# Kernel tuning notes

Measured on AMD Instinct MI355X. Metric: run time of the kernel, lower is better.

The kernel has to match this reference:

```python
import jax, jax.numpy as jnp
import numpy as np

B, S, I, C, H, O = 512, 512, 64, 4, 100, 7


def setup_inputs() -> dict:
    key = jax.random.key(0)
    ks = jax.random.split(key, 4)
    w = lambda k, shape: (jax.random.normal(k, shape, jnp.float32) * 0.05)
    return {
        "x": jax.random.normal(ks[0], (B, S, I), jnp.float32),
        "context_inputs": jnp.ones((C,), jnp.float32) / C,
        "Wf_w": w(ks[1], (H, I + C + H)),
        "Wf_b": jnp.zeros((H,), jnp.float32),
        "Wh_w": w(ks[2], (H, I + C + H)),
        "Wh_b": jnp.zeros((H,), jnp.float32),
        "ro_w": w(ks[3], (O, H)),
        "ro_b": jnp.zeros((O,), jnp.float32),
    }


def reference(x, context_inputs, Wf_w, Wf_b, Wh_w, Wh_b, ro_w, ro_b):
    b, s, i = x.shape
    c = context_inputs.shape[0]
    h_dim = Wf_w.shape[0]
    ic = i + c
    # concatenate the learned context to every timestep (concatenate_context=True path)
    xc = jnp.concatenate([x, jnp.broadcast_to(context_inputs, (b, s, c))], axis=2)
    # split weights into input-driven and hidden-driven parts
    Wf_x, Wf_h = Wf_w[:, :ic], Wf_w[:, ic:]
    Wh_x, Wh_h = Wh_w[:, :ic], Wh_w[:, ic:]
    # precompute all input projections (large GEMMs outside the scan)
    xf = jnp.einsum("bsi,hi->bsh", xc, Wf_x) + Wf_b  # forget-gate input term
    xh = jnp.einsum("bsi,hi->bsh", xc, Wh_x) + Wh_b  # candidate input term

    def step(h, inp):
        xf_t, xh_t = inp  # each (b, h_dim)
        f = jax.nn.sigmoid(xf_t + h @ Wf_h.T)
        h_tilde = jnp.tanh(xh_t + (f * h) @ Wh_h.T)
        h_new = (1.0 - f) * h + f * h_tilde
        return h_new, h_new

    h0 = jnp.zeros((b, h_dim), x.dtype)
    _, hs = jax.lax.scan(step, h0, (xf.transpose(1, 0, 2), xh.transpose(1, 0, 2)))
    hidden_states = hs.transpose(1, 0, 2)  # (b, s, h_dim)
    last_hidden = hidden_states[:, -1, :]
    output = last_hidden @ ro_w.T + ro_b  # (b, O)
    return output, hidden_states
```

## Files before the change

### kernel.cpp

```cpp
#include <hip/hip_runtime.h>

#define NB 512
#define NS 512
#define NI 64
#define NC 4
#define NH 100
#define NO 7
#define IC 68
#define WROW 168
#define KH 112
#define QH 28
#define QX 16

__global__ __launch_bounds__(256, 2) void agent_scan(
    const float* __restrict__ x,
    const float* __restrict__ ctx,
    const float* __restrict__ Wf_w,
    const float* __restrict__ Wf_b,
    const float* __restrict__ Wh_w,
    const float* __restrict__ Wh_b,
    const float* __restrict__ ro_w,
    const float* __restrict__ ro_b,
    float* __restrict__ out)
{
    const int b   = blockIdx.x;
    const int tid = threadIdx.x;
    const int q   = tid & 3;
    const int jj  = tid >> 2;
    const int j0  = 2 * jj;
    const bool act = (jj < NH / 2);

    __shared__ __align__(16) float h_buf[2][KH];
    __shared__ __align__(16) float g_buf[KH];
    __shared__ __align__(16) float x_buf[2][NI];

    for (int i = tid; i < 2 * KH; i += 256) (&h_buf[0][0])[i] = 0.f;
    for (int i = tid; i < KH; i += 256) g_buf[i] = 0.f;

    float wfx[2][QX], whx[2][QX], wfh[2][QH], whh[2][QH];
    float ctxf[2], ctxh[2];
    const float c0 = ctx[0], c1 = ctx[1], c2 = ctx[2], c3 = ctx[3];
    #pragma unroll
    for (int o = 0; o < 2; ++o) {
        const int j = 2 * jj + o;
        if (j < NH) {
            const float* rf = Wf_w + (size_t)j * WROW;
            const float* rh = Wh_w + (size_t)j * WROW;
            #pragma unroll
            for (int i = 0; i < QX; ++i) {
                wfx[o][i] = rf[q * QX + i];
                whx[o][i] = rh[q * QX + i];
            }
            #pragma unroll
            for (int i = 0; i < QH; ++i) {
                const int k = q * QH + i;
                wfh[o][i] = (k < NH) ? rf[IC + k] : 0.f;
                whh[o][i] = (k < NH) ? rh[IC + k] : 0.f;
            }
            ctxf[o] = Wf_b[j] + rf[64] * c0 + rf[65] * c1 + rf[66] * c2 + rf[67] * c3;
            ctxh[o] = Wh_b[j] + rh[64] * c0 + rh[65] * c1 + rh[66] * c2 + rh[67] * c3;
        } else {
            #pragma unroll
            for (int i = 0; i < QX; ++i) { wfx[o][i] = 0.f; whx[o][i] = 0.f; }
            #pragma unroll
            for (int i = 0; i < QH; ++i) { wfh[o][i] = 0.f; whh[o][i] = 0.f; }
            ctxf[o] = 0.f; ctxh[o] = 0.f;
        }
    }

    const float* xrow = x + (size_t)b * NS * NI;
    if (tid < 16) {
        float4 v = *(const float4*)(xrow + tid * 4);
        *(float4*)&x_buf[0][tid * 4] = v;
    }
    __syncthreads();

    float* hid = out + NB * NO + (size_t)b * NS * NH;

    for (int t = 0; t < NS; ++t) {
        const int hb = t & 1;

        float4 xpre = make_float4(0.f, 0.f, 0.f, 0.f);
        if (tid < 16 && t + 1 < NS)
            xpre = *(const float4*)(xrow + (size_t)(t + 1) * NI + tid * 4);

        float pf0 = 0.f, pf1 = 0.f, ph0 = 0.f, ph1 = 0.f;
        #pragma unroll
        for (int u = 0; u < QX; u += 4) {
            const float4 xv = *(const float4*)&x_buf[hb][q * QX + u];
            pf0 += wfx[0][u] * xv.x + wfx[0][u+1] * xv.y + wfx[0][u+2] * xv.z + wfx[0][u+3] * xv.w;
            pf1 += wfx[1][u] * xv.x + wfx[1][u+1] * xv.y + wfx[1][u+2] * xv.z + wfx[1][u+3] * xv.w;
            ph0 += whx[0][u] * xv.x + whx[0][u+1] * xv.y + whx[0][u+2] * xv.z + whx[0][u+3] * xv.w;
            ph1 += whx[1][u] * xv.x + whx[1][u+1] * xv.y + whx[1][u+2] * xv.z + whx[1][u+3] * xv.w;
        }
        float pu0 = 0.f, pu1 = 0.f;
        #pragma unroll
        for (int u = 0; u < QH; u += 4) {
            const float4 hv = *(const float4*)&h_buf[hb][q * QH + u];
            pu0 += wfh[0][u] * hv.x + wfh[0][u+1] * hv.y + wfh[0][u+2] * hv.z + wfh[0][u+3] * hv.w;
            pu1 += wfh[1][u] * hv.x + wfh[1][u+1] * hv.y + wfh[1][u+2] * hv.z + wfh[1][u+3] * hv.w;
        }
        float zf0 = pf0 + pu0, zf1 = pf1 + pu1;
        zf0 += __shfl_xor(zf0, 1); zf0 += __shfl_xor(zf0, 2);
        zf1 += __shfl_xor(zf1, 1); zf1 += __shfl_xor(zf1, 2);
        const float f0 = __fdividef(1.f, 1.f + __expf(-(ctxf[0] + zf0)));
        const float f1 = __fdividef(1.f, 1.f + __expf(-(ctxf[1] + zf1)));

        float hold0 = 0.f, hold1 = 0.f;
        if (act && q == 0) {
            const float2 ho = *(const float2*)&h_buf[hb][j0];
            hold0 = ho.x; hold1 = ho.y;
            float2 g2; g2.x = f0 * hold0; g2.y = f1 * hold1;
            *(float2*)&g_buf[j0] = g2;
        }
        __syncthreads();

        float pv0 = 0.f, pv1 = 0.f;
        #pragma unroll
        for (int u = 0; u < QH; u += 4) {
            const float4 gv = *(const float4*)&g_buf[q * QH + u];
            pv0 += whh[0][u] * gv.x + whh[0][u+1] * gv.y + whh[0][u+2] * gv.z + whh[0][u+3] * gv.w;
            pv1 += whh[1][u] * gv.x + whh[1][u+1] * gv.y + whh[1][u+2] * gv.z + whh[1][u+3] * gv.w;
        }
        float zh0 = ph0 + pv0, zh1 = ph1 + pv1;
        zh0 += __shfl_xor(zh0, 1); zh0 += __shfl_xor(zh0, 2);
        zh1 += __shfl_xor(zh1, 1); zh1 += __shfl_xor(zh1, 2);

        if (act && q == 0) {
            const float e0 = __expf(2.f * (ctxh[0] + zh0));
            const float e1 = __expf(2.f * (ctxh[1] + zh1));
            const float th0 = 1.f - __fdividef(2.f, e0 + 1.f);
            const float th1 = 1.f - __fdividef(2.f, e1 + 1.f);
            const float hn0 = hold0 + f0 * (th0 - hold0);
            const float hn1 = hold1 + f1 * (th1 - hold1);
            *(float2*)&h_buf[hb ^ 1][j0] = make_float2(hn0, hn1);
            *(float2*)&hid[(size_t)t * NH + j0] = make_float2(hn0, hn1);
        }
        if (tid < 16 && t + 1 < NS)
            *(float4*)&x_buf[hb ^ 1][tid * 4] = xpre;
        __syncthreads();
    }

    if (tid < NO) {
        float acc = ro_b[tid];
        const float* rr = ro_w + tid * NH;
        #pragma unroll 4
        for (int i = 0; i < NH; ++i) acc += rr[i] * h_buf[0][i];
        out[b * NO + tid] = acc;
    }
}

extern "C" void kernel_launch(void* const* d_in, const int* in_sizes, int n_in,
                              void* d_out, int out_size, void* d_ws, size_t ws_size,
                              hipStream_t stream) {
    const float* x    = (const float*)d_in[0];
    const float* ctx  = (const float*)d_in[1];
    const float* Wf_w = (const float*)d_in[2];
    const float* Wf_b = (const float*)d_in[3];
    const float* Wh_w = (const float*)d_in[4];
    const float* Wh_b = (const float*)d_in[5];
    const float* ro_w = (const float*)d_in[6];
    const float* ro_b = (const float*)d_in[7];
    (void)in_sizes; (void)n_in; (void)out_size; (void)d_ws; (void)ws_size;
    agent_scan<<<dim3(NB), dim3(256), 0, stream>>>(x, ctx, Wf_w, Wf_b, Wh_w, Wh_b, ro_w, ro_b, (float*)d_out);
}
```

Measured before the change: 850.6 us.

## Pack weights and state as fp16 pairs and use fdot2 for recurrent dot products

Stores weights, inputs and hidden/gated state in fp16 pairs and computes the per-step dot products with packed fdot2 instructions accumulating in fp32. The input and hidden parts are merged into one unified vector layout (x, ctx slot, h) so each gate needs a single contiguous pass. The hidden state is kept in registers rather than re-read from shared memory. This halves register weight storage and the arithmetic instruction count on the serial critical path, but introduces fp16 rounding of weights, inputs and hidden state, which may exceed tolerance across 512 recurrent steps.

```diff
diff --git a/kernel.cpp b/kernel.cpp
--- a/kernel.cpp
+++ b/kernel.cpp
@@ -1,16 +1,28 @@
 #include <hip/hip_runtime.h>
+
+typedef _Float16 half2_t __attribute__((ext_vector_type(2)));
 
 #define NB 512
 #define NS 512
 #define NI 64
-#define NC 4
 #define NH 100
 #define NO 7
-#define IC 68
 #define WROW 168
-#define KH 112
-#define QH 28
-#define QX 16
+#define KP 192
+#define QK 48
+#define QP 24
+
+__device__ __forceinline__ float dot2f(half2_t a, half2_t b, float c) {
+#if defined(__gfx950__) || defined(__gfx942__) || defined(__gfx90a__) || defined(__gfx908__)
+    return __builtin_amdgcn_fdot2(a, b, c, false);
+#else
+    return c + (float)a[0] * (float)b[0] + (float)a[1] * (float)b[1];
+#endif
+}
+
+__device__ __forceinline__ half2_t pack2(float a, float b) {
+    half2_t r; r[0] = (_Float16)a; r[1] = (_Float16)b; return r;
+}
 
 __global__ __launch_bounds__(256, 2) void agent_scan(
     const float* __restrict__ x,
@@ -30,99 +42,104 @@
     const int j0  = 2 * jj;
     const bool act = (jj < NH / 2);
 
-    __shared__ __align__(16) float h_buf[2][KH];
-    __shared__ __align__(16) float g_buf[KH];
-    __shared__ __align__(16) float x_buf[2][NI];
+    __shared__ __align__(16) half2_t vA[2][KP / 2];
+    __shared__ __align__(16) half2_t vC[2][KP / 2];
+    __shared__ float hfin[NH];
 
-    for (int i = tid; i < 2 * KH; i += 256) (&h_buf[0][0])[i] = 0.f;
-    for (int i = tid; i < KH; i += 256) g_buf[i] = 0.f;
+    for (int i = tid; i < KP / 2; i += 256) {
+        half2_t z = pack2(0.f, 0.f);
+        vA[0][i] = z; vA[1][i] = z; vC[0][i] = z; vC[1][i] = z;
+    }
 
-    float wfx[2][QX], whx[2][QX], wfh[2][QH], whh[2][QH];
+    half2_t w[2][2][QP];
     float ctxf[2], ctxh[2];
     const float c0 = ctx[0], c1 = ctx[1], c2 = ctx[2], c3 = ctx[3];
     #pragma unroll
     for (int o = 0; o < 2; ++o) {
-        const int j = 2 * jj + o;
-        if (j < NH) {
-            const float* rf = Wf_w + (size_t)j * WROW;
-            const float* rh = Wh_w + (size_t)j * WROW;
-            #pragma unroll
-            for (int i = 0; i < QX; ++i) {
-                wfx[o][i] = rf[q * QX + i];
-                whx[o][i] = rh[q * QX + i];
-            }
-            #pragma unroll
-            for (int i = 0; i < QH; ++i) {
-                const int k = q * QH + i;
-                wfh[o][i] = (k < NH) ? rf[IC + k] : 0.f;
-                whh[o][i] = (k < NH) ? rh[IC + k] : 0.f;
-            }
-            ctxf[o] = Wf_b[j] + rf[64] * c0 + rf[65] * c1 + rf[66] * c2 + rf[67] * c3;
-            ctxh[o] = Wh_b[j] + rh[64] * c0 + rh[65] * c1 + rh[66] * c2 + rh[67] * c3;
-        } else {
-            #pragma unroll
-            for (int i = 0; i < QX; ++i) { wfx[o][i] = 0.f; whx[o][i] = 0.f; }
-            #pragma unroll
-            for (int i = 0; i < QH; ++i) { wfh[o][i] = 0.f; whh[o][i] = 0.f; }
-            ctxf[o] = 0.f; ctxh[o] = 0.f;
+        const int j = (j0 + o < NH) ? (j0 + o) : (NH - 1);
+        const float* rf = Wf_w + (size_t)j * WROW;
+        const float* rh = Wh_w + (size_t)j * WROW;
+        #pragma unroll
+        for (int u = 0; u < QP; ++u) {
+            const int k  = q * QK + 2 * u;
+            const int kk = (k <= WROW - 2) ? k : 0;
+            const float s = (k <= WROW - 2) ? 1.f : 0.f;
+            w[0][o][u] = pack2(rf[kk] * s, rf[kk + 1] * s);
+            w[1][o][u] = pack2(rh[kk] * s, rh[kk + 1] * s);
         }
+        ctxf[o] = Wf_b[j] + rf[64] * c0 + rf[65] * c1 + rf[66] * c2 + rf[67] * c3;
+        ctxh[o] = Wh_b[j] + rh[64] * c0 + rh[65] * c1 + rh[66] * c2 + rh[67] * c3;
     }
 
     const float* xrow = x + (size_t)b * NS * NI;
     if (tid < 16) {
-        float4 v = *(const float4*)(xrow + tid * 4);
-        *(float4*)&x_buf[0][tid * 4] = v;
+        float4 v4 = *(const float4*)(xrow + tid * 4);
+        half2_t p0 = pack2(v4.x, v4.y), p1 = pack2(v4.z, v4.w);
+        vA[0][2 * tid] = p0; vA[0][2 * tid + 1] = p1;
+        vC[0][2 * tid] = p0; vC[0][2 * tid + 1] = p1;
     }
     __syncthreads();
 
+    float h0 = 0.f, h1 = 0.f;
     float* hid = out + NB * NO + (size_t)b * NS * NH;
 
     for (int t = 0; t < NS; ++t) {
-        const int hb = t & 1;
+        const int cur = t & 1, nxt = cur ^ 1;
 
-        float4 xpre = make_float4(0.f, 0.f, 0.f, 0.f);
+        float4 xp = make_float4(0.f, 0.f, 0.f, 0.f);
         if (tid < 16 && t + 1 < NS)
-            xpre = *(const float4*)(xrow + (size_t)(t + 1) * NI + tid * 4);
+            xp = *(const float4*)(xrow + (size_t)(t + 1) * NI + tid * 4);
 
-        float pf0 = 0.f, pf1 = 0.f, ph0 = 0.f, ph1 = 0.f;
+        uint4 vv[6];
         #pragma unroll
-        for (int u = 0; u < QX; u += 4) {
-            const float4 xv = *(const float4*)&x_buf[hb][q * QX + u];
-            pf0 += wfx[0][u] * xv.x + wfx[0][u+1] * xv.y + wfx[0][u+2] * xv.z + wfx[0][u+3] * xv.w;
-            pf1 += wfx[1][u] * xv.x + wfx[1][u+1] * xv.y + wfx[1][u+2] * xv.z + wfx[1][u+3] * xv.w;
-            ph0 += whx[0][u] * xv.x + whx[0][u+1] * xv.y + whx[0][u+2] * xv.z + whx[0][u+3] * xv.w;
-            ph1 += whx[1][u] * xv.x + whx[1][u+1] * xv.y + whx[1][u+2] * xv.z + whx[1][u+3] * xv.w;
+        for (int r = 0; r < 6; ++r)
+            vv[r] = *(const uint4*)&vA[cur][q * QP + 4 * r];
+        float a0 = 0.f, a0b = 0.f, a1 = 0.f, a1b = 0.f;
+        #pragma unroll
+        for (int r = 0; r < 6; ++r) {
+            half2_t e0 = __builtin_bit_cast(half2_t, vv[r].x);
+            half2_t e1 = __builtin_bit_cast(half2_t, vv[r].y);
+            half2_t e2 = __builtin_bit_cast(half2_t, vv[r].z);
+            half2_t e3 = __builtin_bit_cast(half2_t, vv[r].w);
+            a0  = dot2f(w[0][0][4 * r],     e0, a0);
+            a0b = dot2f(w[0][0][4 * r + 1], e1, a0b);
+            a0  = dot2f(w[0][0][4 * r + 2], e2, a0);
+            a0b = dot2f(w[0][0][4 * r + 3], e3, a0b);
+            a1  = dot2f(w[0][1][4 * r],     e0, a1);
+            a1b = dot2f(w[0][1][4 * r + 1], e1, a1b);
+            a1  = dot2f(w[0][1][4 * r + 2], e2, a1);
+            a1b = dot2f(w[0][1][4 * r + 3], e3, a1b);
         }
-        float pu0 = 0.f, pu1 = 0.f;
-        #pragma unroll
-        for (int u = 0; u < QH; u += 4) {
-            const float4 hv = *(const float4*)&h_buf[hb][q * QH + u];
-            pu0 += wfh[0][u] * hv.x + wfh[0][u+1] * hv.y + wfh[0][u+2] * hv.z + wfh[0][u+3] * hv.w;
-            pu1 += wfh[1][u] * hv.x + wfh[1][u+1] * hv.y + wfh[1][u+2] * hv.z + wfh[1][u+3] * hv.w;
-        }
-        float zf0 = pf0 + pu0, zf1 = pf1 + pu1;
+        float zf0 = a0 + a0b, zf1 = a1 + a1b;
         zf0 += __shfl_xor(zf0, 1); zf0 += __shfl_xor(zf0, 2);
         zf1 += __shfl_xor(zf1, 1); zf1 += __shfl_xor(zf1, 2);
         const float f0 = __fdividef(1.f, 1.f + __expf(-(ctxf[0] + zf0)));
         const float f1 = __fdividef(1.f, 1.f + __expf(-(ctxf[1] + zf1)));
 
-        float hold0 = 0.f, hold1 = 0.f;
-        if (act && q == 0) {
-            const float2 ho = *(const float2*)&h_buf[hb][j0];
-            hold0 = ho.x; hold1 = ho.y;
-            float2 g2; g2.x = f0 * hold0; g2.y = f1 * hold1;
-            *(float2*)&g_buf[j0] = g2;
-        }
+        if (act && q == 0)
+            vC[cur][34 + jj] = pack2(f0 * h0, f1 * h1);
         __syncthreads();
 
-        float pv0 = 0.f, pv1 = 0.f;
         #pragma unroll
-        for (int u = 0; u < QH; u += 4) {
-            const float4 gv = *(const float4*)&g_buf[q * QH + u];
-            pv0 += whh[0][u] * gv.x + whh[0][u+1] * gv.y + whh[0][u+2] * gv.z + whh[0][u+3] * gv.w;
-            pv1 += whh[1][u] * gv.x + whh[1][u+1] * gv.y + whh[1][u+2] * gv.z + whh[1][u+3] * gv.w;
+        for (int r = 0; r < 6; ++r)
+            vv[r] = *(const uint4*)&vC[cur][q * QP + 4 * r];
+        float b0 = 0.f, b0b = 0.f, b1 = 0.f, b1b = 0.f;
+        #pragma unroll
+        for (int r = 0; r < 6; ++r) {
+            half2_t e0 = __builtin_bit_cast(half2_t, vv[r].x);
+            half2_t e1 = __builtin_bit_cast(half2_t, vv[r].y);
+            half2_t e2 = __builtin_bit_cast(half2_t, vv[r].z);
+            half2_t e3 = __builtin_bit_cast(half2_t, vv[r].w);
+            b0  = dot2f(w[1][0][4 * r],     e0, b0);
+            b0b = dot2f(w[1][0][4 * r + 1], e1, b0b);
+            b0  = dot2f(w[1][0][4 * r + 2], e2, b0);
+            b0b = dot2f(w[1][0][4 * r + 3], e3, b0b);
+            b1  = dot2f(w[1][1][4 * r],     e0, b1);
+            b1b = dot2f(w[1][1][4 * r + 1], e1, b1b);
+            b1  = dot2f(w[1][1][4 * r + 2], e2, b1);
+            b1b = dot2f(w[1][1][4 * r + 3], e3, b1b);
         }
-        float zh0 = ph0 + pv0, zh1 = ph1 + pv1;
+        float zh0 = b0 + b0b, zh1 = b1 + b1b;
         zh0 += __shfl_xor(zh0, 1); zh0 += __shfl_xor(zh0, 2);
         zh1 += __shfl_xor(zh1, 1); zh1 += __shfl_xor(zh1, 2);
 
@@ -131,21 +148,26 @@
             const float e1 = __expf(2.f * (ctxh[1] + zh1));
             const float th0 = 1.f - __fdividef(2.f, e0 + 1.f);
             const float th1 = 1.f - __fdividef(2.f, e1 + 1.f);
-            const float hn0 = hold0 + f0 * (th0 - hold0);
-            const float hn1 = hold1 + f1 * (th1 - hold1);
-            *(float2*)&h_buf[hb ^ 1][j0] = make_float2(hn0, hn1);
-            *(float2*)&hid[(size_t)t * NH + j0] = make_float2(hn0, hn1);
+            h0 = h0 + f0 * (th0 - h0);
+            h1 = h1 + f1 * (th1 - h1);
+            *(float2*)&hid[(size_t)t * NH + j0] = make_float2(h0, h1);
+            vA[nxt][34 + jj] = pack2(h0, h1);
         }
-        if (tid < 16 && t + 1 < NS)
-            *(float4*)&x_buf[hb ^ 1][tid * 4] = xpre;
+        if (tid < 16 && t + 1 < NS) {
+            half2_t p0 = pack2(xp.x, xp.y), p1 = pack2(xp.z, xp.w);
+            vA[nxt][2 * tid] = p0; vA[nxt][2 * tid + 1] = p1;
+            vC[nxt][2 * tid] = p0; vC[nxt][2 * tid + 1] = p1;
+        }
         __syncthreads();
     }
 
+    if (act && q == 0) { hfin[j0] = h0; hfin[j0 + 1] = h1; }
+    __syncthreads();
     if (tid < NO) {
         float acc = ro_b[tid];
         const float* rr = ro_w + tid * NH;
         #pragma unroll 4
-        for (int i = 0; i < NH; ++i) acc += rr[i] * h_buf[0][i];
+        for (int i = 0; i < NH; ++i) acc += rr[i] * hfin[i];
         out[b * NO + tid] = acc;
     }
 }
```

After: 821.5 us. 3.4% less time.

## Split input projection into fp16 GEMM kernel and run single-wave fp16 scan

Applied to the files above, without the earlier changes.

Moves the input-side projections (x and context times the input weights) into a separate pre-pass kernel. That kernel writes packed fp16 gate pre-activations into the hidden-state output region as scratch. The recurrent kernel then runs one 64-lane wavefront per batch row, with the recurrent weights packed as fp16 pairs in registers and dot products done by fdot2. Inter-thread syncing relies on LDS wait counts instead of block barriers. This is meant to shorten the per-timestep critical path and remove the x-projection work from the serial loop, at the cost of fp16 rounding of the hidden state, weights and projections, and of relying on wavefront-lockstep ordering.

```diff
diff --git a/kernel.cpp b/kernel.cpp
--- a/kernel.cpp
+++ b/kernel.cpp
@@ -1,152 +1,210 @@
 #include <hip/hip_runtime.h>
+
+typedef _Float16 half2_t __attribute__((ext_vector_type(2)));
 
 #define NB 512
 #define NS 512
 #define NI 64
-#define NC 4
 #define NH 100
 #define NO 7
-#define IC 68
 #define WROW 168
-#define KH 112
+#define KPH 112
 #define QH 28
-#define QX 16
-
-__global__ __launch_bounds__(256, 2) void agent_scan(
-    const float* __restrict__ x,
-    const float* __restrict__ ctx,
-    const float* __restrict__ Wf_w,
-    const float* __restrict__ Wf_b,
-    const float* __restrict__ Wh_w,
-    const float* __restrict__ Wh_b,
-    const float* __restrict__ ro_w,
-    const float* __restrict__ ro_b,
+
+__device__ __forceinline__ float dot2f(half2_t a, half2_t b, float c) {
+    return __builtin_amdgcn_fdot2(a, b, c, false);
+}
+__device__ __forceinline__ half2_t pack2(float a, float b) {
+    half2_t r; r[0] = (_Float16)a; r[1] = (_Float16)b; return r;
+}
+
+__global__ __launch_bounds__(256, 2) void proj_gemm(
+    const float* __restrict__ x, const float* __restrict__ ctx,
+    const float* __restrict__ Wf_w, const float* __restrict__ Wf_b,
+    const float* __restrict__ Wh_w, const float* __restrict__ Wh_b,
     float* __restrict__ out)
 {
-    const int b   = blockIdx.x;
+    __shared__ half2_t wlds[2][NH][36];
+    __shared__ float   blds[2][NH];
     const int tid = threadIdx.x;
-    const int q   = tid & 3;
-    const int jj  = tid >> 2;
-    const int j0  = 2 * jj;
-    const bool act = (jj < NH / 2);
-
-    __shared__ __align__(16) float h_buf[2][KH];
-    __shared__ __align__(16) float g_buf[KH];
-    __shared__ __align__(16) float x_buf[2][NI];
-
-    for (int i = tid; i < 2 * KH; i += 256) (&h_buf[0][0])[i] = 0.f;
-    for (int i = tid; i < KH; i += 256) g_buf[i] = 0.f;
-
-    float wfx[2][QX], whx[2][QX], wfh[2][QH], whh[2][QH];
-    float ctxf[2], ctxh[2];
+
+    for (int idx = tid; idx < 2 * NH * 32; idx += 256) {
+        const int m = idx / (NH * 32), rem = idx % (NH * 32);
+        const int j = rem >> 5, kk = rem & 31;
+        const float* W = m ? Wh_w : Wf_w;
+        wlds[m][j][kk] = pack2(W[j * WROW + 2 * kk], W[j * WROW + 2 * kk + 1]);
+    }
     const float c0 = ctx[0], c1 = ctx[1], c2 = ctx[2], c3 = ctx[3];
+    for (int idx = tid; idx < 2 * NH; idx += 256) {
+        const int m = idx / NH, j = idx % NH;
+        const float* W = m ? Wh_w : Wf_w;
+        const float* Bv = m ? Wh_b : Wf_b;
+        blds[m][j] = Bv[j] + W[j*WROW+64]*c0 + W[j*WROW+65]*c1 + W[j*WROW+66]*c2 + W[j*WROW+67]*c3;
+    }
+    __syncthreads();
+
+    const int rg = tid >> 2, c = tid & 3;
+    const size_t row0 = (size_t)blockIdx.x * 256 + 4 * rg;
+
+    half2_t xv[4][32];
+    const float* xrow = x + row0 * NI;
     #pragma unroll
-    for (int o = 0; o < 2; ++o) {
-        const int j = 2 * jj + o;
-        if (j < NH) {
-            const float* rf = Wf_w + (size_t)j * WROW;
-            const float* rh = Wh_w + (size_t)j * WROW;
-            #pragma unroll
-            for (int i = 0; i < QX; ++i) {
-                wfx[o][i] = rf[q * QX + i];
-                whx[o][i] = rh[q * QX + i];
+    for (int ri = 0; ri < 4; ++ri)
+        #pragma unroll
+        for (int kk = 0; kk < 16; ++kk) {
+            const float4 v = *(const float4*)(xrow + ri * NI + kk * 4);
+            xv[ri][2*kk]   = pack2(v.x, v.y);
+            xv[ri][2*kk+1] = pack2(v.z, v.w);
+        }
+
+    _Float16* opack = (_Float16*)(out + NB * NO);
+    for (int m = 0; m < 2; ++m)
+        for (int o = 0; o < 25; ++o) {
+            const int j = c * 25 + o;
+            half2_t wrow[32];
+            #pragma unroll
+            for (int kk = 0; kk < 32; ++kk) wrow[kk] = wlds[m][j][kk];
+            float a0 = blds[m][j], a1 = a0, a2 = a0, a3 = a0;
+            #pragma unroll
+            for (int kk = 0; kk < 32; ++kk) {
+                a0 = dot2f(wrow[kk], xv[0][kk], a0);
+                a1 = dot2f(wrow[kk], xv[1][kk], a1);
+                a2 = dot2f(wrow[kk], xv[2][kk], a2);
+                a3 = dot2f(wrow[kk], xv[3][kk], a3);
             }
-            #pragma unroll
-            for (int i = 0; i < QH; ++i) {
-                const int k = q * QH + i;
-                wfh[o][i] = (k < NH) ? rf[IC + k] : 0.f;
-                whh[o][i] = (k < NH) ? rh[IC + k] : 0.f;
-            }
-            ctxf[o] = Wf_b[j] + rf[64] * c0 + rf[65] * c1 + rf[66] * c2 + rf[67] * c3;
-            ctxh[o] = Wh_b[j] + rh[64] * c0 + rh[65] * c1 + rh[66] * c2 + rh[67] * c3;
-        } else {
-            #pragma unroll
-            for (int i = 0; i < QX; ++i) { wfx[o][i] = 0.f; whx[o][i] = 0.f; }
-            #pragma unroll
-            for (int i = 0; i < QH; ++i) { wfh[o][i] = 0.f; whh[o][i] = 0.f; }
-            ctxf[o] = 0.f; ctxh[o] = 0.f;
-        }
-    }
-
-    const float* xrow = x + (size_t)b * NS * NI;
-    if (tid < 16) {
-        float4 v = *(const float4*)(xrow + tid * 4);
-        *(float4*)&x_buf[0][tid * 4] = v;
-    }
-    __syncthreads();
-
-    float* hid = out + NB * NO + (size_t)b * NS * NH;
+            _Float16* op = opack + row0 * 200 + m * NH + j;
+            op[0]   = (_Float16)a0;
+            op[200] = (_Float16)a1;
+            op[400] = (_Float16)a2;
+            op[600] = (_Float16)a3;
+        }
+}
+
+__global__ __launch_bounds__(64, 1) void agent_scan(
+    const float* __restrict__ Wf_w, const float* __restrict__ Wh_w,
+    const float* __restrict__ ro_w, const float* __restrict__ ro_b,
+    float* __restrict__ out)
+{
+    const int b    = blockIdx.x;
+    const int lane = threadIdx.x;
+    const int g    = lane >> 2, q = lane & 3;
+
+    __shared__ __align__(16) _Float16 vh[KPH];
+    __shared__ __align__(16) _Float16 vg[KPH];
+    __shared__ float hfin[NH];
+
+    for (int i = lane; i < KPH; i += 64) { vh[i] = (_Float16)0.f; vg[i] = (_Float16)0.f; }
+
+    half2_t wf[7][14], wh[7][14];
+    #pragma unroll
+    for (int o = 0; o < 7; ++o) {
+        const int j = 7 * g + o;
+        const bool v = (j < NH);
+        const int jc = v ? j : NH - 1;
+        const float* rf = Wf_w + (size_t)jc * WROW + 68;
+        const float* rh = Wh_w + (size_t)jc * WROW + 68;
+        #pragma unroll
+        for (int u = 0; u < 14; ++u) {
+            const int k0 = QH * q + 2 * u, k1 = k0 + 1;
+            const float f0 = (v && k0 < NH) ? rf[k0] : 0.f;
+            const float f1 = (v && k1 < NH) ? rf[k1] : 0.f;
+            const float g0 = (v && k0 < NH) ? rh[k0] : 0.f;
+            const float g1 = (v && k1 < NH) ? rh[k1] : 0.f;
+            wf[o][u] = pack2(f0, f1);
+            wh[o][u] = pack2(g0, g1);
+        }
+    }
+
+    const int jA = 7 * g + q;
+    const int jB = 7 * g + 4 + q;
+    const bool hasA = (jA < NH);
+    const bool hasB = (q < 3) && (jB < NH);
+    const int jAc = hasA ? jA : 0;
+    const int jBc = hasB ? jB : 0;
+    const int oB  = (q < 3) ? 4 + q : 0;
+
+    const unsigned short* pux = (const unsigned short*)(out + NB * NO) + (size_t)b * NS * 200;
+    float* hidbase = out + NB * NO + (size_t)b * NS * NH;
+
+    float hA = 0.f, hB = 0.f;
+    unsigned short uA0 = pux[jAc], uB0 = pux[jBc];
+    unsigned short uA1 = pux[NH + jAc], uB1 = pux[NH + jBc];
+
+    __asm__ volatile("s_waitcnt lgkmcnt(0)" ::: "memory");
 
     for (int t = 0; t < NS; ++t) {
-        const int hb = t & 1;
-
-        float4 xpre = make_float4(0.f, 0.f, 0.f, 0.f);
-        if (tid < 16 && t + 1 < NS)
-            xpre = *(const float4*)(xrow + (size_t)(t + 1) * NI + tid * 4);
-
-        float pf0 = 0.f, pf1 = 0.f, ph0 = 0.f, ph1 = 0.f;
-        #pragma unroll
-        for (int u = 0; u < QX; u += 4) {
-            const float4 xv = *(const float4*)&x_buf[hb][q * QX + u];
-            pf0 += wfx[0][u] * xv.x + wfx[0][u+1] * xv.y + wfx[0][u+2] * xv.z + wfx[0][u+3] * xv.w;
-            pf1 += wfx[1][u] * xv.x + wfx[1][u+1] * xv.y + wfx[1][u+2] * xv.z + wfx[1][u+3] * xv.w;
-            ph0 += whx[0][u] * xv.x + whx[0][u+1] * xv.y + whx[0][u+2] * xv.z + whx[0][u+3] * xv.w;
-            ph1 += whx[1][u] * xv.x + whx[1][u+1] * xv.y + whx[1][u+2] * xv.z + whx[1][u+3] * xv.w;
-        }
-        float pu0 = 0.f, pu1 = 0.f;
-        #pragma unroll
-        for (int u = 0; u < QH; u += 4) {
-            const float4 hv = *(const float4*)&h_buf[hb][q * QH + u];
-            pu0 += wfh[0][u] * hv.x + wfh[0][u+1] * hv.y + wfh[0][u+2] * hv.z + wfh[0][u+3] * hv.w;
-            pu1 += wfh[1][u] * hv.x + wfh[1][u+1] * hv.y + wfh[1][u+2] * hv.z + wfh[1][u+3] * hv.w;
-        }
-        float zf0 = pf0 + pu0, zf1 = pf1 + pu1;
-        zf0 += __shfl_xor(zf0, 1); zf0 += __shfl_xor(zf0, 2);
-        zf1 += __shfl_xor(zf1, 1); zf1 += __shfl_xor(zf1, 2);
-        const float f0 = __fdividef(1.f, 1.f + __expf(-(ctxf[0] + zf0)));
-        const float f1 = __fdividef(1.f, 1.f + __expf(-(ctxf[1] + zf1)));
-
-        float hold0 = 0.f, hold1 = 0.f;
-        if (act && q == 0) {
-            const float2 ho = *(const float2*)&h_buf[hb][j0];
-            hold0 = ho.x; hold1 = ho.y;
-            float2 g2; g2.x = f0 * hold0; g2.y = f1 * hold1;
-            *(float2*)&g_buf[j0] = g2;
-        }
-        __syncthreads();
-
-        float pv0 = 0.f, pv1 = 0.f;
-        #pragma unroll
-        for (int u = 0; u < QH; u += 4) {
-            const float4 gv = *(const float4*)&g_buf[q * QH + u];
-            pv0 += whh[0][u] * gv.x + whh[0][u+1] * gv.y + whh[0][u+2] * gv.z + whh[0][u+3] * gv.w;
-            pv1 += whh[1][u] * gv.x + whh[1][u+1] * gv.y + whh[1][u+2] * gv.z + whh[1][u+3] * gv.w;
-        }
-        float zh0 = ph0 + pv0, zh1 = ph1 + pv1;
-        zh0 += __shfl_xor(zh0, 1); zh0 += __shfl_xor(zh0, 2);
-        zh1 += __shfl_xor(zh1, 1); zh1 += __shfl_xor(zh1, 2);
-
-        if (act && q == 0) {
-            const float e0 = __expf(2.f * (ctxh[0] + zh0));
-            const float e1 = __expf(2.f * (ctxh[1] + zh1));
-            const float th0 = 1.f - __fdividef(2.f, e0 + 1.f);
-            const float th1 = 1.f - __fdividef(2.f, e1 + 1.f);
-            const float hn0 = hold0 + f0 * (th0 - hold0);
-            const float hn1 = hold1 + f1 * (th1 - hold1);
-            *(float2*)&h_buf[hb ^ 1][j0] = make_float2(hn0, hn1);
-            *(float2*)&hid[(size_t)t * NH + j0] = make_float2(hn0, hn1);
-        }
-        if (tid < 16 && t + 1 < NS)
-            *(float4*)&x_buf[hb ^ 1][tid * 4] = xpre;
-        __syncthreads();
-    }
-
-    if (tid < NO) {
-        float acc = ro_b[tid];
-        const float* rr = ro_w + tid * NH;
+        const unsigned short* nr = pux + (size_t)((t + 1 < NS) ? t + 1 : t) * 200;
+        const unsigned short nA0 = nr[jAc], nB0 = nr[jBc];
+        const unsigned short nA1 = nr[NH + jAc], nB1 = nr[NH + jBc];
+
+        float acc[7] = {0.f, 0.f, 0.f, 0.f, 0.f, 0.f, 0.f};
+        {
+            const half2_t* ph = (const half2_t*)(vh + QH * q);
+            half2_t p[14];
+            #pragma unroll
+            for (int u = 0; u < 14; ++u) p[u] = ph[u];
+            #pragma unroll
+            for (int o = 0; o < 7; ++o)
+                #pragma unroll
+                for (int u = 0; u < 14; ++u) acc[o] = dot2f(wf[o][u], p[u], acc[o]);
+        }
+        #pragma unroll
+        for (int o = 0; o < 7; ++o) {
+            float s = acc[o];
+            s += __shfl_xor(s, 1); s += __shfl_xor(s, 2);
+            acc[o] = s;
+        }
+        const float xfA = (float)__builtin_bit_cast(_Float16, uA0);
+        const float xfB = (float)__builtin_bit_cast(_Float16, uB0);
+        const float fA = __fdividef(1.f, 1.f + __expf(-(xfA + acc[q])));
+        const float fB = __fdividef(1.f, 1.f + __expf(-(xfB + acc[oB])));
+        if (hasA) vg[jA] = (_Float16)(fA * hA);
+        if (hasB) vg[jB] = (_Float16)(fB * hB);
+        __asm__ volatile("s_waitcnt lgkmcnt(0)" ::: "memory");
+
+        #pragma unroll
+        for (int o = 0; o < 7; ++o) acc[o] = 0.f;
+        {
+            const half2_t* pg = (const half2_t*)(vg + QH * q);
+            half2_t p[14];
+            #pragma unroll
+            for (int u = 0; u < 14; ++u) p[u] = pg[u];
+            #pragma unroll
+            for (int o = 0; o < 7; ++o)
+                #pragma unroll
+                for (int u = 0; u < 14; ++u) acc[o] = dot2f(wh[o][u], p[u], acc[o]);
+        }
+        #pragma unroll
+        for (int o = 0; o < 7; ++o) {
+            float s = acc[o];
+            s += __shfl_xor(s, 1); s += __shfl_xor(s, 2);
+            acc[o] = s;
+        }
+        const float xhA = (float)__builtin_bit_cast(_Float16, uA1);
+        const float xhB = (float)__builtin_bit_cast(_Float16, uB1);
+        const float eA = __expf(2.f * (xhA + acc[q]));
+        const float eB = __expf(2.f * (xhB + acc[oB]));
+        const float thA = 1.f - __fdividef(2.f, eA + 1.f);
+        const float thB = 1.f - __fdividef(2.f, eB + 1.f);
+        hA = hA + fA * (thA - hA);
+        hB = hB + fB * (thB - hB);
+
+        float* hrow = hidbase + (size_t)t * NH;
+        if (hasA) { vh[jA] = (_Float16)hA; hrow[jA] = hA; }
+        if (hasB) { vh[jB] = (_Float16)hB; hrow[jB] = hB; }
+        uA0 = nA0; uB0 = nB0; uA1 = nA1; uB1 = nB1;
+        __asm__ volatile("s_waitcnt lgkmcnt(0)" ::: "memory");
+    }
+
+    if (hasA) hfin[jA] = hA;
+    if (hasB) hfin[jB] = hB;
+    __asm__ volatile("s_waitcnt lgkmcnt(0)" ::: "memory");
+    if (lane < NO) {
+        float acc = ro_b[lane];
+        const float* rr = ro_w + lane * NH;
         #pragma unroll 4
-        for (int i = 0; i < NH; ++i) acc += rr[i] * h_buf[0][i];
-        out[b * NO + tid] = acc;
+        for (int i = 0; i < NH; ++i) acc += rr[i] * hfin[i];
+        out[b * NO + lane] = acc;
     }
 }
 
@@ -162,5 +220,8 @@
     const float* ro_w = (const float*)d_in[6];
     const float* ro_b = (const float*)d_in[7];
     (void)in_sizes; (void)n_in; (void)out_size; (void)d_ws; (void)ws_size;
-    agent_scan<<<dim3(NB), dim3(256), 0, stream>>>(x, ctx, Wf_w, Wf_b, Wh_w, Wh_b, ro_w, ro_b, (float*)d_out);
-}
+    float* out = (float*)d_out;
+
+    proj_gemm<<<dim3((NB * NS) / 256), dim3(256), 0, stream>>>(x, ctx, Wf_w, Wf_b, Wh_w, Wh_b, out);
+    agent_scan<<<dim3(NB), dim3(64), 0, stream>>>(Wf_w, Wh_w, ro_w, ro_b, out);
+}
```

Result: slower. 1.183 ms (+39.0%).

## Run each batch scan in a single wavefront with fp16 packed dot2 math

Applied to the files above, without the earlier changes.

Each batch row now runs in one 64-lane wavefront instead of a 256-thread block. Every lane holds full weight rows as packed fp16 pairs and uses v_dot2 instructions. Because the block is a single wave, __syncthreads and the cross-lane shuffle reductions are gone, and LDS ordering relies on compiler barriers only. This removes per-step barrier and reduction latency from the serial recurrence and halves ALU work. The costs are fp16 rounding of weights, inputs and hidden state inside the recurrence, which may breach tolerance over 512 steps, and very high register pressure (~264 VGPRs for weights) with only 512 waves total.

```diff
diff --git a/kernel.cpp b/kernel.cpp
--- a/kernel.cpp
+++ b/kernel.cpp
@@ -1,18 +1,28 @@
 #include <hip/hip_runtime.h>
+
+typedef _Float16 half2_t __attribute__((ext_vector_type(2)));
 
 #define NB 512
 #define NS 512
 #define NI 64
-#define NC 4
 #define NH 100
 #define NO 7
-#define IC 68
 #define WROW 168
-#define KH 112
-#define QH 28
-#define QX 16
 
-__global__ __launch_bounds__(256, 2) void agent_scan(
+__device__ __forceinline__ float dot2f(half2_t a, half2_t b, float c) {
+    return __builtin_amdgcn_fdot2(a, b, c, false);
+}
+__device__ __forceinline__ half2_t pack2(float a, float b) {
+    half2_t r; r[0] = (_Float16)a; r[1] = (_Float16)b; return r;
+}
+__device__ __forceinline__ unsigned pack2u(float a, float b) {
+    return __builtin_bit_cast(unsigned, pack2(a, b));
+}
+__device__ __forceinline__ half2_t h2(unsigned u) {
+    return __builtin_bit_cast(half2_t, u);
+}
+
+__global__ __launch_bounds__(64, 1) void agent_scan(
     const float* __restrict__ x,
     const float* __restrict__ ctx,
     const float* __restrict__ Wf_w,
@@ -23,130 +33,152 @@
     const float* __restrict__ ro_b,
     float* __restrict__ out)
 {
-    const int b   = blockIdx.x;
-    const int tid = threadIdx.x;
-    const int q   = tid & 3;
-    const int jj  = tid >> 2;
-    const int j0  = 2 * jj;
-    const bool act = (jj < NH / 2);
+    const int b = blockIdx.x, lane = threadIdx.x;
+    const int j0 = 2 * lane;
+    const bool act = (lane < NH / 2);
 
-    __shared__ __align__(16) float h_buf[2][KH];
-    __shared__ __align__(16) float g_buf[KH];
-    __shared__ __align__(16) float x_buf[2][NI];
+    __shared__ __align__(16) unsigned vx[32];
+    __shared__ __align__(16) unsigned vh[52];
+    __shared__ __align__(16) unsigned vg[52];
+    __shared__ __align__(16) float hfin[NH];
 
-    for (int i = tid; i < 2 * KH; i += 256) (&h_buf[0][0])[i] = 0.f;
-    for (int i = tid; i < KH; i += 256) g_buf[i] = 0.f;
+    if (lane < 52) { vh[lane] = 0u; vg[lane] = 0u; }
 
-    float wfx[2][QX], whx[2][QX], wfh[2][QH], whh[2][QH];
-    float ctxf[2], ctxh[2];
+    const float s = act ? 1.f : 0.f;
+    const int jc0 = act ? j0 : 0;
+    half2_t wfx[2][32], whx[2][32], wfh[2][50], whh[2][50];
+    float cf[2], ch[2];
     const float c0 = ctx[0], c1 = ctx[1], c2 = ctx[2], c3 = ctx[3];
     #pragma unroll
     for (int o = 0; o < 2; ++o) {
-        const int j = 2 * jj + o;
-        if (j < NH) {
-            const float* rf = Wf_w + (size_t)j * WROW;
-            const float* rh = Wh_w + (size_t)j * WROW;
-            #pragma unroll
-            for (int i = 0; i < QX; ++i) {
-                wfx[o][i] = rf[q * QX + i];
-                whx[o][i] = rh[q * QX + i];
-            }
-            #pragma unroll
-            for (int i = 0; i < QH; ++i) {
-                const int k = q * QH + i;
-                wfh[o][i] = (k < NH) ? rf[IC + k] : 0.f;
-                whh[o][i] = (k < NH) ? rh[IC + k] : 0.f;
-            }
-            ctxf[o] = Wf_b[j] + rf[64] * c0 + rf[65] * c1 + rf[66] * c2 + rf[67] * c3;
-            ctxh[o] = Wh_b[j] + rh[64] * c0 + rh[65] * c1 + rh[66] * c2 + rh[67] * c3;
-        } else {
-            #pragma unroll
-            for (int i = 0; i < QX; ++i) { wfx[o][i] = 0.f; whx[o][i] = 0.f; }
-            #pragma unroll
-            for (int i = 0; i < QH; ++i) { wfh[o][i] = 0.f; whh[o][i] = 0.f; }
-            ctxf[o] = 0.f; ctxh[o] = 0.f;
+        const float* rf = Wf_w + (size_t)(jc0 + o) * WROW;
+        const float* rh = Wh_w + (size_t)(jc0 + o) * WROW;
+        #pragma unroll
+        for (int u = 0; u < 16; ++u) {
+            const float4 a  = *(const float4*)(rf + 4 * u);
+            const float4 bb = *(const float4*)(rh + 4 * u);
+            wfx[o][2*u]   = pack2(s * a.x,  s * a.y);
+            wfx[o][2*u+1] = pack2(s * a.z,  s * a.w);
+            whx[o][2*u]   = pack2(s * bb.x, s * bb.y);
+            whx[o][2*u+1] = pack2(s * bb.z, s * bb.w);
         }
+        #pragma unroll
+        for (int u = 0; u < 25; ++u) {
+            const float4 a  = *(const float4*)(rf + 68 + 4 * u);
+            const float4 bb = *(const float4*)(rh + 68 + 4 * u);
+            wfh[o][2*u]   = pack2(s * a.x,  s * a.y);
+            wfh[o][2*u+1] = pack2(s * a.z,  s * a.w);
+            whh[o][2*u]   = pack2(s * bb.x, s * bb.y);
+            whh[o][2*u+1] = pack2(s * bb.z, s * bb.w);
+        }
+        const float4 cfv = *(const float4*)(rf + 64);
+        const float4 chv = *(const float4*)(rh + 64);
+        cf[o] = Wf_b[jc0+o] + cfv.x*c0 + cfv.y*c1 + cfv.z*c2 + cfv.w*c3;
+        ch[o] = Wh_b[jc0+o] + chv.x*c0 + chv.y*c1 + chv.z*c2 + chv.w*c3;
     }
 
     const float* xrow = x + (size_t)b * NS * NI;
-    if (tid < 16) {
-        float4 v = *(const float4*)(xrow + tid * 4);
-        *(float4*)&x_buf[0][tid * 4] = v;
+    float4 xp = make_float4(0.f, 0.f, 0.f, 0.f);
+    if (lane < 16) {
+        const float4 v = *(const float4*)(xrow + 4 * lane);
+        *(uint2*)&vx[2*lane] = make_uint2(pack2u(v.x, v.y), pack2u(v.z, v.w));
+        xp = *(const float4*)(xrow + NI + 4 * lane);
     }
-    __syncthreads();
+    asm volatile("" ::: "memory");
 
-    float* hid = out + NB * NO + (size_t)b * NS * NH;
+    float* hidbase = out + NB * NO + (size_t)b * NS * NH;
+    float h0 = 0.f, h1 = 0.f;
 
     for (int t = 0; t < NS; ++t) {
-        const int hb = t & 1;
+        half2_t xb[32];
+        #pragma unroll
+        for (int r = 0; r < 8; ++r) {
+            const uint4 v = *(const uint4*)&vx[4*r];
+            xb[4*r] = h2(v.x); xb[4*r+1] = h2(v.y); xb[4*r+2] = h2(v.z); xb[4*r+3] = h2(v.w);
+        }
+        half2_t hb[52];
+        #pragma unroll
+        for (int r = 0; r < 13; ++r) {
+            const uint4 v = *(const uint4*)&vh[4*r];
+            hb[4*r] = h2(v.x); hb[4*r+1] = h2(v.y); hb[4*r+2] = h2(v.z); hb[4*r+3] = h2(v.w);
+        }
+        asm volatile("" ::: "memory");
+        if (lane < 16)
+            *(uint2*)&vx[2*lane] = make_uint2(pack2u(xp.x, xp.y), pack2u(xp.z, xp.w));
+        {
+            const int tn = (t + 2 < NS) ? t + 2 : NS - 1;
+            if (lane < 16) xp = *(const float4*)(xrow + (size_t)tn * NI + 4 * lane);
+        }
 
-        float4 xpre = make_float4(0.f, 0.f, 0.f, 0.f);
-        if (tid < 16 && t + 1 < NS)
-            xpre = *(const float4*)(xrow + (size_t)(t + 1) * NI + tid * 4);
+        float af0=0.f, af1=0.f, ag0=0.f, ag1=0.f;
+        float ah0=0.f, ah1=0.f, ai0=0.f, ai1=0.f;
+        #pragma unroll
+        for (int u = 0; u < 32; u += 2) {
+            af0 = dot2f(wfx[0][u],   xb[u],   af0);
+            af1 = dot2f(wfx[0][u+1], xb[u+1], af1);
+            ag0 = dot2f(wfx[1][u],   xb[u],   ag0);
+            ag1 = dot2f(wfx[1][u+1], xb[u+1], ag1);
+            ah0 = dot2f(whx[0][u],   xb[u],   ah0);
+            ah1 = dot2f(whx[0][u+1], xb[u+1], ah1);
+            ai0 = dot2f(whx[1][u],   xb[u],   ai0);
+            ai1 = dot2f(whx[1][u+1], xb[u+1], ai1);
+        }
+        float bf0=0.f, bf1=0.f, bg0=0.f, bg1=0.f;
+        #pragma unroll
+        for (int u = 0; u < 50; u += 2) {
+            bf0 = dot2f(wfh[0][u],   hb[u],   bf0);
+            bf1 = dot2f(wfh[0][u+1], hb[u+1], bf1);
+            bg0 = dot2f(wfh[1][u],   hb[u],   bg0);
+            bg1 = dot2f(wfh[1][u+1], hb[u+1], bg1);
+        }
+        const float zf0 = cf[0] + af0 + af1 + bf0 + bf1;
+        const float zf1 = cf[1] + ag0 + ag1 + bg0 + bg1;
+        const float f0 = __fdividef(1.f, 1.f + __expf(-zf0));
+        const float f1 = __fdividef(1.f, 1.f + __expf(-zf1));
 
-        float pf0 = 0.f, pf1 = 0.f, ph0 = 0.f, ph1 = 0.f;
+        if (act) vg[lane] = pack2u(f0 * h0, f1 * h1);
+        asm volatile("" ::: "memory");
+
+        half2_t gb[52];
         #pragma unroll
-        for (int u = 0; u < QX; u += 4) {
-            const float4 xv = *(const float4*)&x_buf[hb][q * QX + u];
-            pf0 += wfx[0][u] * xv.x + wfx[0][u+1] * xv.y + wfx[0][u+2] * xv.z + wfx[0][u+3] * xv.w;
-            pf1 += wfx[1][u] * xv.x + wfx[1][u+1] * xv.y + wfx[1][u+2] * xv.z + wfx[1][u+3] * xv.w;
-            ph0 += whx[0][u] * xv.x + whx[0][u+1] * xv.y + whx[0][u+2] * xv.z + whx[0][u+3] * xv.w;
-            ph1 += whx[1][u] * xv.x + whx[1][u+1] * xv.y + whx[1][u+2] * xv.z + whx[1][u+3] * xv.w;
+        for (int r = 0; r < 13; ++r) {
+            const uint4 v = *(const uint4*)&vg[4*r];
+            gb[4*r] = h2(v.x); gb[4*r+1] = h2(v.y); gb[4*r+2] = h2(v.z); gb[4*r+3] = h2(v.w);
         }
-        float pu0 = 0.f, pu1 = 0.f;
+        float bh0=0.f, bh1=0.f, bi0=0.f, bi1=0.f;
         #pragma unroll
-        for (int u = 0; u < QH; u += 4) {
-            const float4 hv = *(const float4*)&h_buf[hb][q * QH + u];
-            pu0 += wfh[0][u] * hv.x + wfh[0][u+1] * hv.y + wfh[0][u+2] * hv.z + wfh[0][u+3] * hv.w;
-            pu1 += wfh[1][u] * hv.x + wfh[1][u+1] * hv.y + wfh[1][u+2] * hv.z + wfh[1][u+3] * hv.w;
+        for (int u = 0; u < 50; u += 2) {
+            bh0 = dot2f(whh[0][u],   gb[u],   bh0);
+            bh1 = dot2f(whh[0][u+1], gb[u+1], bh1);
+            bi0 = dot2f(whh[1][u],   gb[u],   bi0);
+            bi1 = dot2f(whh[1][u+1], gb[u+1], bi1);
         }
-        float zf0 = pf0 + pu0, zf1 = pf1 + pu1;
-        zf0 += __shfl_xor(zf0, 1); zf0 += __shfl_xor(zf0, 2);
-        zf1 += __shfl_xor(zf1, 1); zf1 += __shfl_xor(zf1, 2);
-        const float f0 = __fdividef(1.f, 1.f + __expf(-(ctxf[0] + zf0)));
-        const float f1 = __fdividef(1.f, 1.f + __expf(-(ctxf[1] + zf1)));
+        const float zh0 = ch[0] + ah0 + ah1 + bh0 + bh1;
+        const float zh1 = ch[1] + ai0 + ai1 + bi0 + bi1;
+        const float e0 = __expf(2.f * zh0), e1 = __expf(2.f * zh1);
+        const float th0 = 1.f - __fdividef(2.f, e0 + 1.f);
+        const float th1 = 1.f - __fdividef(2.f, e1 + 1.f);
+        h0 += f0 * (th0 - h0);
+        h1 += f1 * (th1 - h1);
 
-        float hold0 = 0.f, hold1 = 0.f;
-        if (act && q == 0) {
-            const float2 ho = *(const float2*)&h_buf[hb][j0];
-            hold0 = ho.x; hold1 = ho.y;
-            float2 g2; g2.x = f0 * hold0; g2.y = f1 * hold1;
-            *(float2*)&g_buf[j0] = g2;
+        if (act) {
+            vh[lane] = pack2u(h0, h1);
+            *(float2*)(hidbase + (size_t)t * NH + j0) = make_float2(h0, h1);
         }
-        __syncthreads();
-
-        float pv0 = 0.f, pv1 = 0.f;
-        #pragma unroll
-        for (int u = 0; u < QH; u += 4) {
-            const float4 gv = *(const float4*)&g_buf[q * QH + u];
-            pv0 += whh[0][u] * gv.x + whh[0][u+1] * gv.y + whh[0][u+2] * gv.z + whh[0][u+3] * gv.w;
-            pv1 += whh[1][u] * gv.x + whh[1][u+1] * gv.y + whh[1][u+2] * gv.z + whh[1][u+3] * gv.w;
-        }
-        float zh0 = ph0 + pv0, zh1 = ph1 + pv1;
-        zh0 += __shfl_xor(zh0, 1); zh0 += __shfl_xor(zh0, 2);
-        zh1 += __shfl_xor(zh1, 1); zh1 += __shfl_xor(zh1, 2);
-
-        if (act && q == 0) {
-            const float e0 = __expf(2.f * (ctxh[0] + zh0));
-            const float e1 = __expf(2.f * (ctxh[1] + zh1));
-            const float th0 = 1.f - __fdividef(2.f, e0 + 1.f);
-            const float th1 = 1.f - __fdividef(2.f, e1 + 1.f);
-            const float hn0 = hold0 + f0 * (th0 - hold0);
-            const float hn1 = hold1 + f1 * (th1 - hold1);
-            *(float2*)&h_buf[hb ^ 1][j0] = make_float2(hn0, hn1);
-            *(float2*)&hid[(size_t)t * NH + j0] = make_float2(hn0, hn1);
-        }
-        if (tid < 16 && t + 1 < NS)
-            *(float4*)&x_buf[hb ^ 1][tid * 4] = xpre;
-        __syncthreads();
+        asm volatile("" ::: "memory");
     }
 
-    if (tid < NO) {
-        float acc = ro_b[tid];
-        const float* rr = ro_w + tid * NH;
-        #pragma unroll 4
-        for (int i = 0; i < NH; ++i) acc += rr[i] * h_buf[0][i];
-        out[b * NO + tid] = acc;
+    if (act) *(float2*)&hfin[j0] = make_float2(h0, h1);
+    asm volatile("" ::: "memory");
+    if (lane < NO) {
+        float acc = ro_b[lane];
+        const float* rr = ro_w + lane * NH;
+        #pragma unroll
+        for (int u = 0; u < 25; ++u) {
+            const float4 v = *(const float4*)(rr + 4 * u);
+            acc += v.x * hfin[4*u] + v.y * hfin[4*u+1] + v.z * hfin[4*u+2] + v.w * hfin[4*u+3];
+        }
+        out[b * NO + lane] = acc;
     }
 }
 
@@ -162,5 +194,5 @@
     const float* ro_w = (const float*)d_in[6];
     const float* ro_b = (const float*)d_in[7];
     (void)in_sizes; (void)n_in; (void)out_size; (void)d_ws; (void)ws_size;
-    agent_scan<<<dim3(NB), dim3(256), 0, stream>>>(x, ctx, Wf_w, Wf_b, Wh_w, Wh_b, ro_w, ro_b, (float*)d_out);
+    agent_scan<<<dim3(NB), dim3(64), 0, stream>>>(x, ctx, Wf_w, Wf_b, Wh_w, Wh_b, ro_w, ro_b, (float*)d_out);
 }
```

Measured after the change: 880.3 us. 3.5% more time.
